# Performance work log

Measured on AMD Instinct MI355X. Metric: run time of the kernel, lower is better.

## Reference

```python
import jax, jax.numpy as jnp
import numpy as np
import math

B, N, K, C = 2, 8192, 16, 64
PE_DIM, HID = 32, 16
SIGMA, EPS = 1.0, 1e-06


def setup_inputs() -> dict:
    key = jax.random.key(0)
    ks = jax.random.split(key, 8)
    p = jax.random.normal(ks[0], (B, N, 3), jnp.float32)
    f = jax.random.normal(ks[1], (B, C, N), jnp.float32)
    pe = jax.random.normal(ks[2], (B, C, N, K), jnp.float32)
    knn_idx = jax.random.randint(ks[3], (B, N, K), 0, N, jnp.int32)
    # LocalAggregation convs1: 1x1 conv [C -> C] (+ReLU)
    W1 = jax.random.normal(ks[4], (C, C), jnp.float32) * (1.0 / math.sqrt(C))
    b1 = jnp.zeros((C,), jnp.float32)
    # GaussianKDEOffsetGenerator params: pe_mlp Linear(3->32), ffn Linear(32->16)->Linear(16->3)
    Wpe = jax.random.normal(ks[5], (PE_DIM, 3), jnp.float32) * (1.0 / math.sqrt(3))
    bpe = jnp.zeros((PE_DIM,), jnp.float32)
    Wh1 = jax.random.normal(ks[6], (HID, PE_DIM), jnp.float32) * (1.0 / math.sqrt(PE_DIM))
    bh1 = jnp.zeros((HID,), jnp.float32)
    Wh2 = jax.random.normal(ks[7], (3, HID), jnp.float32) * (1.0 / math.sqrt(HID))
    bh2 = jnp.zeros((3,), jnp.float32)
    return {"p": p, "f": f, "pe": pe, "W1": W1, "b1": b1, "Wpe": Wpe,
            "bpe": bpe, "Wh1": Wh1, "bh1": bh1, "Wh2": Wh2, "bh2": bh2,
            "knn_idx": knn_idx}


def reference(p, f, pe, W1, b1, Wpe, bpe, Wh1, bh1, Wh2, bh2, knn_idx):
    gather = jax.vmap(lambda a, i: a[i])  # per-batch neighbor gather
    # --- LocalAggregation: convs1 (1x1 conv + relu), group_by_idx, pe+fj, max-pool over K ---
    h = jax.nn.relu(jnp.einsum('oc,bcn->bon', W1, f) + b1[None, :, None])  # [B,C,N]
    ht = jnp.transpose(h, (0, 2, 1))                                       # [B,N,C]
    fj = gather(ht, knn_idx)                                               # [B,N,K,C]
    fout = jnp.max(pe + jnp.transpose(fj, (0, 3, 1, 2)), axis=-1)          # [B,C,N]
    # --- GaussianKDEOffsetGenerator on grouped neighbor coords [B*N, K, 3] ---
    coords = gather(p, knn_idx).reshape(B * N, K, 3)
    rel = coords[:, :, None, :] - coords[:, None, :, :]                    # [BN,K,K,3]
    pek = jax.nn.relu(jnp.einsum('nijc,dc->nijd', rel, Wpe) + bpe).mean(axis=2)  # [BN,K,PE]
    dist2 = jnp.sum(rel * rel, axis=-1)                                    # [BN,K,K]
    coef = 1.0 / math.sqrt(2.0 * math.pi * SIGMA ** 2 + EPS)
    kde = (coef * jnp.exp(-dist2 / (2.0 * SIGMA ** 2 + EPS))).sum(axis=2, keepdims=True)
    kde = kde / (jnp.max(kde, axis=1, keepdims=True) + EPS)                # [BN,K,1]
    fused = pek * kde
    delta = jax.nn.relu(fused @ Wh1.T + bh1) @ Wh2.T + bh2                 # [BN,K,3]
    return (fout, delta)
```

## Files before the change

### kernel.cpp

```cpp
#include <hip/hip_runtime.h>

#define B_ 2
#define N_ 8192
#define K_ 16
#define C_ 64
#define PE_ 32
#define HID_ 16

typedef float f4 __attribute__((ext_vector_type(4)));

__device__ __forceinline__ f4 splat4(float x) { f4 r = {x, x, x, x}; return r; }
__device__ __forceinline__ f4 relu4(f4 v) {
  f4 r;
  r[0] = fmaxf(v[0], 0.f); r[1] = fmaxf(v[1], 0.f);
  r[2] = fmaxf(v[2], 0.f); r[3] = fmaxf(v[3], 0.f);
  return r;
}
__device__ __forceinline__ float dot4(float4 w, f4 v) {
  return fmaf(w.x, v[0], fmaf(w.y, v[1], fmaf(w.z, v[2], w.w * v[3])));
}

struct PK4 { f4 k0, k1, k2, k3; };

__device__ __forceinline__ PK4 channel(const float4* __restrict__ sq,
                                       int d, const float* __restrict__ Wpe,
                                       const float* __restrict__ bpe) {
  const float wx = Wpe[d * 3 + 0], wy = Wpe[d * 3 + 1], wz = Wpe[d * 3 + 2];
  const float wb = bpe[d];
  const float4 A0 = sq[0], B0 = sq[1], C0 = sq[2];
  const float4 A1 = sq[3], B1 = sq[4], C1 = sq[5];
  const float4 A2 = sq[6], B2 = sq[7], C2 = sq[8];
  const float4 A3 = sq[9], B3 = sq[10], C3 = sq[11];
  const float p0  = fmaf(wx, A0.x, fmaf(wy, A0.y, wz * A0.z));
  const float p1  = fmaf(wx, A0.w, fmaf(wy, B0.x, wz * B0.y));
  const float p2  = fmaf(wx, B0.z, fmaf(wy, B0.w, wz * C0.x));
  const float p3  = fmaf(wx, C0.y, fmaf(wy, C0.z, wz * C0.w));
  const float p4  = fmaf(wx, A1.x, fmaf(wy, A1.y, wz * A1.z));
  const float p5  = fmaf(wx, A1.w, fmaf(wy, B1.x, wz * B1.y));
  const float p6  = fmaf(wx, B1.z, fmaf(wy, B1.w, wz * C1.x));
  const float p7  = fmaf(wx, C1.y, fmaf(wy, C1.z, wz * C1.w));
  const float p8  = fmaf(wx, A2.x, fmaf(wy, A2.y, wz * A2.z));
  const float p9  = fmaf(wx, A2.w, fmaf(wy, B2.x, wz * B2.y));
  const float p10 = fmaf(wx, B2.z, fmaf(wy, B2.w, wz * C2.x));
  const float p11 = fmaf(wx, C2.y, fmaf(wy, C2.z, wz * C2.w));
  const float p12 = fmaf(wx, A3.x, fmaf(wy, A3.y, wz * A3.z));
  const float p13 = fmaf(wx, A3.w, fmaf(wy, B3.x, wz * B3.y));
  const float p14 = fmaf(wx, B3.z, fmaf(wy, B3.w, wz * C3.x));
  const float p15 = fmaf(wx, C3.y, fmaf(wy, C3.z, wz * C3.w));
  const f4 a0 = {p0 + wb, p1 + wb, p2 + wb, p3 + wb};
  const f4 a1 = {p4 + wb, p5 + wb, p6 + wb, p7 + wb};
  const f4 a2 = {p8 + wb, p9 + wb, p10 + wb, p11 + wb};
  const f4 a3 = {p12 + wb, p13 + wb, p14 + wb, p15 + wb};
  f4 k0 = splat4(0.f), k1 = splat4(0.f), k2 = splat4(0.f), k3 = splat4(0.f);
#define KSTEP(PJ)                                  \
  {                                                \
    const f4 sp = splat4(PJ);                      \
    k0 += relu4(a0 - sp); k1 += relu4(a1 - sp);    \
    k2 += relu4(a2 - sp); k3 += relu4(a3 - sp);    \
  }
  KSTEP(p0) KSTEP(p1) KSTEP(p2) KSTEP(p3) KSTEP(p4) KSTEP(p5) KSTEP(p6)
  KSTEP(p7) KSTEP(p8) KSTEP(p9) KSTEP(p10) KSTEP(p11) KSTEP(p12) KSTEP(p13)
  KSTEP(p14) KSTEP(p15)
#undef KSTEP
  PK4 r; r.k0 = k0; r.k1 = k1; r.k2 = k2; r.k3 = k3;
  return r;
}

__global__ __launch_bounds__(256) void k1_conv(
    const float* __restrict__ f, const float* __restrict__ W1,
    const float* __restrict__ b1, float* __restrict__ ht) {
  const int t = threadIdx.x;
  const int lane = t & 63;
  const int w = t >> 6;
  const int g0 = blockIdx.x * 16 + w * 4;
  const int b = g0 >> 13;
  const int n = g0 & (N_ - 1);
  const f4* wp = reinterpret_cast<const f4*>(W1 + lane * C_);
  const f4 w0 = wp[0], w1 = wp[1], w2 = wp[2], w3 = wp[3];
  const f4 w4 = wp[4], w5 = wp[5], w6 = wp[6], w7 = wp[7];
  const f4 w8 = wp[8], w9 = wp[9], w10 = wp[10], w11 = wp[11];
  const f4 w12 = wp[12], w13 = wp[13], w14 = wp[14], w15 = wp[15];
  const float* fb = f + (size_t)b * C_ * N_ + n;
  f4 a = splat4(0.f);
#define CSTEP(Q, E)                                                        \
  {                                                                        \
    const f4 fv = *reinterpret_cast<const f4*>(fb + (size_t)(Q * 4 + E) * N_); \
    a += splat4(w##Q[E]) * fv;                                             \
  }
#define CQ(Q) CSTEP(Q, 0) CSTEP(Q, 1) CSTEP(Q, 2) CSTEP(Q, 3)
  CQ(0) CQ(1) CQ(2) CQ(3) CQ(4) CQ(5) CQ(6) CQ(7)
  CQ(8) CQ(9) CQ(10) CQ(11) CQ(12) CQ(13) CQ(14) CQ(15)
#undef CQ
#undef CSTEP
  const float bias = b1[lane];
  #pragma unroll
  for (int pt = 0; pt < 4; ++pt)
    ht[(size_t)(b * N_ + n + pt) * C_ + lane] = fmaxf(a[pt] + bias, 0.f);
}

#define SFJ_STRIDE 65
#define SOUT_OFF 16640
#define NP2 1024
__global__ __launch_bounds__(256) void k23_split(
    const float* __restrict__ p, const float* __restrict__ pe,
    const float* __restrict__ ht, const int* __restrict__ knn,
    const float* __restrict__ Wpe, const float* __restrict__ bpe,
    const float* __restrict__ Wh1, const float* __restrict__ bh1,
    const float* __restrict__ Wh2, const float* __restrict__ bh2,
    float* __restrict__ fout, float* __restrict__ delta) {
  __shared__ __align__(16) char smem[21760];
  const int t = threadIdx.x;

  if (blockIdx.x < NP2) {
    float* sfj = (float*)smem;
    float* sout = (float*)(smem + SOUT_OFF);
    const int base = blockIdx.x * 16;
    const int b = base >> 13;
    const int n0b = base & (N_ - 1);
    const int lane = t & 63;
    const int w = t >> 6;
    const int csub = lane >> 4, sl = lane & 15;
    const int j = sl & 3, nn = sl >> 2;
    #pragma unroll 1
    for (int si = 0; si < 4; ++si) {
      const int n0 = n0b + si * 4;
      #pragma unroll
      for (int n = 0; n < 4; ++n) {
        const int* kn = knn + (size_t)(b * N_ + n0 + n) * K_ + w * 4;
        #pragma unroll
        for (int kk = 0; kk < 4; ++kk) {
          const int id = kn[kk];
          const float hv = ht[(size_t)(b * N_ + id) * C_ + lane];
          sfj[lane * SFJ_STRIDE + (n * 4 + w) * 4 + kk] = hv;
        }
      }
      __syncthreads();
      #pragma unroll
      for (int it2 = 0; it2 < 4; ++it2) {
        const int c = it2 * 16 + w * 4 + csub;
        const f4 pv = __builtin_nontemporal_load(
            reinterpret_cast<const f4*>(pe + ((size_t)(b * C_ + c) * N_ + n0) * K_) + sl);
        const f4 fj = *reinterpret_cast<const f4*>(&sfj[c * SFJ_STRIDE + sl * 4]);
        float v = fmaxf(fmaxf(pv[0] + fj[0], pv[1] + fj[1]),
                        fmaxf(pv[2] + fj[2], pv[3] + fj[3]));
        v = fmaxf(v, __shfl_xor(v, 1));
        v = fmaxf(v, __shfl_xor(v, 2));
        if (j == 0) sout[c * 20 + si * 4 + nn] = v;
      }
      __syncthreads();
    }
    const int c = t >> 2, q = t & 3;
    const float4 r = *reinterpret_cast<const float4*>(&sout[c * 20 + q * 4]);
    *reinterpret_cast<float4*>(fout + (size_t)(b * C_ + c) * N_ + n0b + q * 4) = r;
    return;
  }

  {
    float* spk = (float*)smem;
    float* sc = (float*)(smem + 16384);
    const int base = (blockIdx.x - NP2) * 8;
    const int b = base >> 13;
    const int g = t >> 5;
    const int l = t & 31;

    if (l < 16) {
      const int gid = base + g;
      const int idx = knn[(size_t)gid * K_ + l];
      const float* pp = p + (size_t)(b * N_ + idx) * 3;
      sc[g * 48 + l * 3 + 0] = pp[0];
      sc[g * 48 + l * 3 + 1] = pp[1];
      sc[g * 48 + l * 3 + 2] = pp[2];
    }
    __syncthreads();

    {
      const int d = l;
      const float4* sq = reinterpret_cast<const float4*>(&sc[g * 48]);
      const PK4 ck = channel(sq, d, Wpe, bpe);
      const int qw = d >> 2, pos = d & 3;
      float* gbase = spk + g * 512;
#define PKW(II, KV) \
      gbase[(II) * 32 + (((qw ^ ((II) & 7)) << 2) | pos)] = ck.KV[(II) & 3];
      PKW(0, k0) PKW(1, k0) PKW(2, k0) PKW(3, k0)
      PKW(4, k1) PKW(5, k1) PKW(6, k1) PKW(7, k1)
      PKW(8, k2) PKW(9, k2) PKW(10, k2) PKW(11, k2)
      PKW(12, k3) PKW(13, k3) PKW(14, k3) PKW(15, k3)
#undef PKW
    }
    __syncthreads();

    {
      const int i = t & 15, half = (t >> 4) & 1;
      const int gid = base + g;
      const float ci0 = sc[g * 48 + i * 3 + 0];
      const float ci1 = sc[g * 48 + i * 3 + 1];
      const float ci2 = sc[g * 48 + i * 3 + 2];
      const float4* sq = reinterpret_cast<const float4*>(&sc[g * 48]);
      const float INV2S = 0.49999975f;
      const float COEF = 0.39894225f;
      float kacc = 0.f;
      #pragma unroll
      for (int jj = 0; jj < 2; ++jj) {
        const int j4 = half * 2 + jj;
        const float4 a = sq[j4 * 3 + 0], b4 = sq[j4 * 3 + 1], c4 = sq[j4 * 3 + 2];
        float dx, dy, dz;
        dx = ci0 - a.x;  dy = ci1 - a.y;  dz = ci2 - a.z;
        kacc += __expf(-(dx * dx + dy * dy + dz * dz) * INV2S);
        dx = ci0 - a.w;  dy = ci1 - b4.x; dz = ci2 - b4.y;
        kacc += __expf(-(dx * dx + dy * dy + dz * dz) * INV2S);
        dx = ci0 - b4.z; dy = ci1 - b4.w; dz = ci2 - c4.x;
        kacc += __expf(-(dx * dx + dy * dy + dz * dz) * INV2S);
        dx = ci0 - c4.y; dy = ci1 - c4.z; dz = ci2 - c4.w;
        kacc += __expf(-(dx * dx + dy * dy + dz * dz) * INV2S);
      }
      kacc += __shfl_xor(kacc, 16);
      const float kde = COEF * kacc;
      float m = kde;
      m = fmaxf(m, __shfl_xor(m, 1));
      m = fmaxf(m, __shfl_xor(m, 2));
      m = fmaxf(m, __shfl_xor(m, 4));
      m = fmaxf(m, __shfl_xor(m, 8));
      const float s = (kde / (m + 1e-6f)) * (1.f / 16.f);

      const float* rbase = spk + g * 512 + i * 32;
      const int ix = i & 7;
      const f4 v0 = *reinterpret_cast<const f4*>(&rbase[(0 ^ ix) << 2]);
      const f4 v1 = *reinterpret_cast<const f4*>(&rbase[(1 ^ ix) << 2]);
      const f4 v2 = *reinterpret_cast<const f4*>(&rbase[(2 ^ ix) << 2]);
      const f4 v3 = *reinterpret_cast<const f4*>(&rbase[(3 ^ ix) << 2]);
      const f4 v4 = *reinterpret_cast<const f4*>(&rbase[(4 ^ ix) << 2]);
      const f4 v5 = *reinterpret_cast<const f4*>(&rbase[(5 ^ ix) << 2]);
      const f4 v6 = *reinterpret_cast<const f4*>(&rbase[(6 ^ ix) << 2]);
      const f4 v7 = *reinterpret_cast<const f4*>(&rbase[(7 ^ ix) << 2]);

      float o0 = 0.f, o1 = 0.f, o2 = 0.f;
      #pragma unroll
      for (int hh = 0; hh < 8; ++hh) {
        const int h = half * 8 + hh;
        const float4* Wr = reinterpret_cast<const float4*>(Wh1 + h * PE_);
        const float u = dot4(Wr[0], v0) + dot4(Wr[1], v1) + dot4(Wr[2], v2) +
                        dot4(Wr[3], v3) + dot4(Wr[4], v4) + dot4(Wr[5], v5) +
                        dot4(Wr[6], v6) + dot4(Wr[7], v7);
        const float a = fmaxf(fmaf(s, u, bh1[h]), 0.f);
        o0 = fmaf(Wh2[0 * HID_ + h], a, o0);
        o1 = fmaf(Wh2[1 * HID_ + h], a, o1);
        o2 = fmaf(Wh2[2 * HID_ + h], a, o2);
      }
      o0 += __shfl_xor(o0, 16);
      o1 += __shfl_xor(o1, 16);
      o2 += __shfl_xor(o2, 16);
      if (half == 0) {
        float* dp = delta + ((size_t)gid * K_ + i) * 3;
        dp[0] = o0 + bh2[0];
        dp[1] = o1 + bh2[1];
        dp[2] = o2 + bh2[2];
      }
    }
  }
}

extern "C" void kernel_launch(void* const* d_in, const int* in_sizes, int n_in,
                              void* d_out, int out_size, void* d_ws, size_t ws_size,
                              hipStream_t stream) {
  const float* p   = (const float*)d_in[0];
  const float* f   = (const float*)d_in[1];
  const float* pe  = (const float*)d_in[2];
  const float* W1  = (const float*)d_in[3];
  const float* b1  = (const float*)d_in[4];
  const float* Wpe = (const float*)d_in[5];
  const float* bpe = (const float*)d_in[6];
  const float* Wh1 = (const float*)d_in[7];
  const float* bh1 = (const float*)d_in[8];
  const float* Wh2 = (const float*)d_in[9];
  const float* bh2 = (const float*)d_in[10];
  const int* knn   = (const int*)d_in[11];
  float* fout  = (float*)d_out;
  float* delta = (float*)d_out + (size_t)B_ * C_ * N_;
  float* ht = (float*)d_ws;

  k1_conv<<<(B_ * N_) / 16, 256, 0, stream>>>(f, W1, b1, ht);
  k23_split<<<NP2 + (B_ * N_) / 8, 256, 0, stream>>>(
      p, pe, ht, knn, Wpe, bpe, Wh1, bh1, Wh2, bh2, fout, delta);
}
```

Measured before the change: 65.99 us.

## Split KDE offset work across conv and gather kernels to balance launches

Restructures the two launches so the independent KDE/offset-MLP blocks are split between the first kernel (with the 1x1 conv) and the second kernel (with the neighbor gather and max-pool). The goal is to fill the conv kernel, which is lighter and bandwidth-bound, with compute work that does not depend on its output. That shortens the second kernel's tail. The first kernel now also allocates shared memory for the KDE blocks, and the fixed split ratio may not match the actual costs of each phase.

```diff
diff --git a/kernel.cpp b/kernel.cpp
--- a/kernel.cpp
+++ b/kernel.cpp
@@ -66,13 +66,12 @@
   return r;
 }
 
-__global__ __launch_bounds__(256) void k1_conv(
-    const float* __restrict__ f, const float* __restrict__ W1,
+__device__ __forceinline__ void k1_body(
+    int blk, int t, const float* __restrict__ f, const float* __restrict__ W1,
     const float* __restrict__ b1, float* __restrict__ ht) {
-  const int t = threadIdx.x;
   const int lane = t & 63;
   const int w = t >> 6;
-  const int g0 = blockIdx.x * 16 + w * 4;
+  const int g0 = blk * 16 + w * 4;
   const int b = g0 >> 13;
   const int n = g0 & (N_ - 1);
   const f4* wp = reinterpret_cast<const f4*>(W1 + lane * C_);
@@ -100,163 +99,193 @@
 
 #define SFJ_STRIDE 65
 #define SOUT_OFF 16640
-#define NP2 1024
-__global__ __launch_bounds__(256) void k23_split(
-    const float* __restrict__ p, const float* __restrict__ pe,
+__device__ __forceinline__ void p2_body(
+    char* smem, int blk, int t, const float* __restrict__ pe,
     const float* __restrict__ ht, const int* __restrict__ knn,
+    float* __restrict__ fout) {
+  float* sfj = (float*)smem;
+  float* sout = (float*)(smem + SOUT_OFF);
+  const int base = blk * 16;
+  const int b = base >> 13;
+  const int n0b = base & (N_ - 1);
+  const int lane = t & 63;
+  const int w = t >> 6;
+  const int csub = lane >> 4, sl = lane & 15;
+  const int j = sl & 3, nn = sl >> 2;
+  #pragma unroll 1
+  for (int si = 0; si < 4; ++si) {
+    const int n0 = n0b + si * 4;
+    #pragma unroll
+    for (int n = 0; n < 4; ++n) {
+      const int* kn = knn + (size_t)(b * N_ + n0 + n) * K_ + w * 4;
+      #pragma unroll
+      for (int kk = 0; kk < 4; ++kk) {
+        const int id = kn[kk];
+        const float hv = ht[(size_t)(b * N_ + id) * C_ + lane];
+        sfj[lane * SFJ_STRIDE + (n * 4 + w) * 4 + kk] = hv;
+      }
+    }
+    __syncthreads();
+    #pragma unroll
+    for (int it2 = 0; it2 < 4; ++it2) {
+      const int c = it2 * 16 + w * 4 + csub;
+      const f4 pv = __builtin_nontemporal_load(
+          reinterpret_cast<const f4*>(pe + ((size_t)(b * C_ + c) * N_ + n0) * K_) + sl);
+      const f4 fj = *reinterpret_cast<const f4*>(&sfj[c * SFJ_STRIDE + sl * 4]);
+      float v = fmaxf(fmaxf(pv[0] + fj[0], pv[1] + fj[1]),
+                      fmaxf(pv[2] + fj[2], pv[3] + fj[3]));
+      v = fmaxf(v, __shfl_xor(v, 1));
+      v = fmaxf(v, __shfl_xor(v, 2));
+      if (j == 0) sout[c * 20 + si * 4 + nn] = v;
+    }
+    __syncthreads();
+  }
+  const int c = t >> 2, q = t & 3;
+  const float4 r = *reinterpret_cast<const float4*>(&sout[c * 20 + q * 4]);
+  *reinterpret_cast<float4*>(fout + (size_t)(b * C_ + c) * N_ + n0b + q * 4) = r;
+}
+
+__device__ __forceinline__ void p3_body(
+    char* smem, int base, int t, const float* __restrict__ p,
+    const int* __restrict__ knn, const float* __restrict__ Wpe,
+    const float* __restrict__ bpe, const float* __restrict__ Wh1,
+    const float* __restrict__ bh1, const float* __restrict__ Wh2,
+    const float* __restrict__ bh2, float* __restrict__ delta) {
+  float* spk = (float*)smem;
+  float* sc = (float*)(smem + 16384);
+  const int b = base >> 13;
+  const int g = t >> 5;
+  const int l = t & 31;
+
+  if (l < 16) {
+    const int gid = base + g;
+    const int idx = knn[(size_t)gid * K_ + l];
+    const float* pp = p + (size_t)(b * N_ + idx) * 3;
+    sc[g * 48 + l * 3 + 0] = pp[0];
+    sc[g * 48 + l * 3 + 1] = pp[1];
+    sc[g * 48 + l * 3 + 2] = pp[2];
+  }
+  __syncthreads();
+
+  {
+    const int d = l;
+    const float4* sq = reinterpret_cast<const float4*>(&sc[g * 48]);
+    const PK4 ck = channel(sq, d, Wpe, bpe);
+    const int qw = d >> 2, pos = d & 3;
+    float* gbase = spk + g * 512;
+#define PKW(II, KV) \
+    gbase[(II) * 32 + (((qw ^ ((II) & 7)) << 2) | pos)] = ck.KV[(II) & 3];
+    PKW(0, k0) PKW(1, k0) PKW(2, k0) PKW(3, k0)
+    PKW(4, k1) PKW(5, k1) PKW(6, k1) PKW(7, k1)
+    PKW(8, k2) PKW(9, k2) PKW(10, k2) PKW(11, k2)
+    PKW(12, k3) PKW(13, k3) PKW(14, k3) PKW(15, k3)
+#undef PKW
+  }
+  __syncthreads();
+
+  {
+    const int i = t & 15, half = (t >> 4) & 1;
+    const int gid = base + g;
+    const float ci0 = sc[g * 48 + i * 3 + 0];
+    const float ci1 = sc[g * 48 + i * 3 + 1];
+    const float ci2 = sc[g * 48 + i * 3 + 2];
+    const float4* sq = reinterpret_cast<const float4*>(&sc[g * 48]);
+    const float INV2S = 0.49999975f;
+    const float COEF = 0.39894225f;
+    float kacc = 0.f;
+    #pragma unroll
+    for (int jj = 0; jj < 2; ++jj) {
+      const int j4 = half * 2 + jj;
+      const float4 a = sq[j4 * 3 + 0], b4 = sq[j4 * 3 + 1], c4 = sq[j4 * 3 + 2];
+      float dx, dy, dz;
+      dx = ci0 - a.x;  dy = ci1 - a.y;  dz = ci2 - a.z;
+      kacc += __expf(-(dx * dx + dy * dy + dz * dz) * INV2S);
+      dx = ci0 - a.w;  dy = ci1 - b4.x; dz = ci2 - b4.y;
+      kacc += __expf(-(dx * dx + dy * dy + dz * dz) * INV2S);
+      dx = ci0 - b4.z; dy = ci1 - b4.w; dz = ci2 - c4.x;
+      kacc += __expf(-(dx * dx + dy * dy + dz * dz) * INV2S);
+      dx = ci0 - c4.y; dy = ci1 - c4.z; dz = ci2 - c4.w;
+      kacc += __expf(-(dx * dx + dy * dy + dz * dz) * INV2S);
+    }
+    kacc += __shfl_xor(kacc, 16);
+    const float kde = COEF * kacc;
+    float m = kde;
+    m = fmaxf(m, __shfl_xor(m, 1));
+    m = fmaxf(m, __shfl_xor(m, 2));
+    m = fmaxf(m, __shfl_xor(m, 4));
+    m = fmaxf(m, __shfl_xor(m, 8));
+    const float s = (kde / (m + 1e-6f)) * (1.f / 16.f);
+
+    const float* rbase = spk + g * 512 + i * 32;
+    const int ix = i & 7;
+    const f4 v0 = *reinterpret_cast<const f4*>(&rbase[(0 ^ ix) << 2]);
+    const f4 v1 = *reinterpret_cast<const f4*>(&rbase[(1 ^ ix) << 2]);
+    const f4 v2 = *reinterpret_cast<const f4*>(&rbase[(2 ^ ix) << 2]);
+    const f4 v3 = *reinterpret_cast<const f4*>(&rbase[(3 ^ ix) << 2]);
+    const f4 v4 = *reinterpret_cast<const f4*>(&rbase[(4 ^ ix) << 2]);
+    const f4 v5 = *reinterpret_cast<const f4*>(&rbase[(5 ^ ix) << 2]);
+    const f4 v6 = *reinterpret_cast<const f4*>(&rbase[(6 ^ ix) << 2]);
+    const f4 v7 = *reinterpret_cast<const f4*>(&rbase[(7 ^ ix) << 2]);
+
+    float o0 = 0.f, o1 = 0.f, o2 = 0.f;
+    #pragma unroll
+    for (int hh = 0; hh < 8; ++hh) {
+      const int h = half * 8 + hh;
+      const float4* Wr = reinterpret_cast<const float4*>(Wh1 + h * PE_);
+      const float u = dot4(Wr[0], v0) + dot4(Wr[1], v1) + dot4(Wr[2], v2) +
+                      dot4(Wr[3], v3) + dot4(Wr[4], v4) + dot4(Wr[5], v5) +
+                      dot4(Wr[6], v6) + dot4(Wr[7], v7);
+      const float a = fmaxf(fmaf(s, u, bh1[h]), 0.f);
+      o0 = fmaf(Wh2[0 * HID_ + h], a, o0);
+      o1 = fmaf(Wh2[1 * HID_ + h], a, o1);
+      o2 = fmaf(Wh2[2 * HID_ + h], a, o2);
+    }
+    o0 += __shfl_xor(o0, 16);
+    o1 += __shfl_xor(o1, 16);
+    o2 += __shfl_xor(o2, 16);
+    if (half == 0) {
+      float* dp = delta + ((size_t)gid * K_ + i) * 3;
+      dp[0] = o0 + bh2[0];
+      dp[1] = o1 + bh2[1];
+      dp[2] = o2 + bh2[2];
+    }
+  }
+}
+
+#define NP3A 1280
+__global__ __launch_bounds__(256) void kA(
+    const float* __restrict__ f, const float* __restrict__ W1,
+    const float* __restrict__ b1, float* __restrict__ ht,
+    const float* __restrict__ p, const int* __restrict__ knn,
     const float* __restrict__ Wpe, const float* __restrict__ bpe,
     const float* __restrict__ Wh1, const float* __restrict__ bh1,
     const float* __restrict__ Wh2, const float* __restrict__ bh2,
-    float* __restrict__ fout, float* __restrict__ delta) {
+    float* __restrict__ delta) {
+  __shared__ __align__(16) char smem[17920];
+  const int t = threadIdx.x;
+  if (blockIdx.x < 1024) {
+    k1_body(blockIdx.x, t, f, W1, b1, ht);
+    return;
+  }
+  p3_body(smem, (blockIdx.x - 1024) * 8, t, p, knn, Wpe, bpe, Wh1, bh1,
+          Wh2, bh2, delta);
+}
+
+__global__ __launch_bounds__(256) void kB(
+    const float* __restrict__ pe, const float* __restrict__ ht,
+    const int* __restrict__ knn, float* __restrict__ fout,
+    const float* __restrict__ p, const float* __restrict__ Wpe,
+    const float* __restrict__ bpe, const float* __restrict__ Wh1,
+    const float* __restrict__ bh1, const float* __restrict__ Wh2,
+    const float* __restrict__ bh2, float* __restrict__ delta) {
   __shared__ __align__(16) char smem[21760];
   const int t = threadIdx.x;
-
-  if (blockIdx.x < NP2) {
-    float* sfj = (float*)smem;
-    float* sout = (float*)(smem + SOUT_OFF);
-    const int base = blockIdx.x * 16;
-    const int b = base >> 13;
-    const int n0b = base & (N_ - 1);
-    const int lane = t & 63;
-    const int w = t >> 6;
-    const int csub = lane >> 4, sl = lane & 15;
-    const int j = sl & 3, nn = sl >> 2;
-    #pragma unroll 1
-    for (int si = 0; si < 4; ++si) {
-      const int n0 = n0b + si * 4;
-      #pragma unroll
-      for (int n = 0; n < 4; ++n) {
-        const int* kn = knn + (size_t)(b * N_ + n0 + n) * K_ + w * 4;
-        #pragma unroll
-        for (int kk = 0; kk < 4; ++kk) {
-          const int id = kn[kk];
-          const float hv = ht[(size_t)(b * N_ + id) * C_ + lane];
-          sfj[lane * SFJ_STRIDE + (n * 4 + w) * 4 + kk] = hv;
-        }
-      }
-      __syncthreads();
-      #pragma unroll
-      for (int it2 = 0; it2 < 4; ++it2) {
-        const int c = it2 * 16 + w * 4 + csub;
-        const f4 pv = __builtin_nontemporal_load(
-            reinterpret_cast<const f4*>(pe + ((size_t)(b * C_ + c) * N_ + n0) * K_) + sl);
-        const f4 fj = *reinterpret_cast<const f4*>(&sfj[c * SFJ_STRIDE + sl * 4]);
-        float v = fmaxf(fmaxf(pv[0] + fj[0], pv[1] + fj[1]),
-                        fmaxf(pv[2] + fj[2], pv[3] + fj[3]));
-        v = fmaxf(v, __shfl_xor(v, 1));
-        v = fmaxf(v, __shfl_xor(v, 2));
-        if (j == 0) sout[c * 20 + si * 4 + nn] = v;
-      }
-      __syncthreads();
-    }
-    const int c = t >> 2, q = t & 3;
-    const float4 r = *reinterpret_cast<const float4*>(&sout[c * 20 + q * 4]);
-    *reinterpret_cast<float4*>(fout + (size_t)(b * C_ + c) * N_ + n0b + q * 4) = r;
+  if (blockIdx.x < 1024) {
+    p2_body(smem, blockIdx.x, t, pe, ht, knn, fout);
     return;
   }
-
-  {
-    float* spk = (float*)smem;
-    float* sc = (float*)(smem + 16384);
-    const int base = (blockIdx.x - NP2) * 8;
-    const int b = base >> 13;
-    const int g = t >> 5;
-    const int l = t & 31;
-
-    if (l < 16) {
-      const int gid = base + g;
-      const int idx = knn[(size_t)gid * K_ + l];
-      const float* pp = p + (size_t)(b * N_ + idx) * 3;
-      sc[g * 48 + l * 3 + 0] = pp[0];
-      sc[g * 48 + l * 3 + 1] = pp[1];
-      sc[g * 48 + l * 3 + 2] = pp[2];
-    }
-    __syncthreads();
-
-    {
-      const int d = l;
-      const float4* sq = reinterpret_cast<const float4*>(&sc[g * 48]);
-      const PK4 ck = channel(sq, d, Wpe, bpe);
-      const int qw = d >> 2, pos = d & 3;
-      float* gbase = spk + g * 512;
-#define PKW(II, KV) \
-      gbase[(II) * 32 + (((qw ^ ((II) & 7)) << 2) | pos)] = ck.KV[(II) & 3];
-      PKW(0, k0) PKW(1, k0) PKW(2, k0) PKW(3, k0)
-      PKW(4, k1) PKW(5, k1) PKW(6, k1) PKW(7, k1)
-      PKW(8, k2) PKW(9, k2) PKW(10, k2) PKW(11, k2)
-      PKW(12, k3) PKW(13, k3) PKW(14, k3) PKW(15, k3)
-#undef PKW
-    }
-    __syncthreads();
-
-    {
-      const int i = t & 15, half = (t >> 4) & 1;
-      const int gid = base + g;
-      const float ci0 = sc[g * 48 + i * 3 + 0];
-      const float ci1 = sc[g * 48 + i * 3 + 1];
-      const float ci2 = sc[g * 48 + i * 3 + 2];
-      const float4* sq = reinterpret_cast<const float4*>(&sc[g * 48]);
-      const float INV2S = 0.49999975f;
-      const float COEF = 0.39894225f;
-      float kacc = 0.f;
-      #pragma unroll
-      for (int jj = 0; jj < 2; ++jj) {
-        const int j4 = half * 2 + jj;
-        const float4 a = sq[j4 * 3 + 0], b4 = sq[j4 * 3 + 1], c4 = sq[j4 * 3 + 2];
-        float dx, dy, dz;
-        dx = ci0 - a.x;  dy = ci1 - a.y;  dz = ci2 - a.z;
-        kacc += __expf(-(dx * dx + dy * dy + dz * dz) * INV2S);
-        dx = ci0 - a.w;  dy = ci1 - b4.x; dz = ci2 - b4.y;
-        kacc += __expf(-(dx * dx + dy * dy + dz * dz) * INV2S);
-        dx = ci0 - b4.z; dy = ci1 - b4.w; dz = ci2 - c4.x;
-        kacc += __expf(-(dx * dx + dy * dy + dz * dz) * INV2S);
-        dx = ci0 - c4.y; dy = ci1 - c4.z; dz = ci2 - c4.w;
-        kacc += __expf(-(dx * dx + dy * dy + dz * dz) * INV2S);
-      }
-      kacc += __shfl_xor(kacc, 16);
-      const float kde = COEF * kacc;
-      float m = kde;
-      m = fmaxf(m, __shfl_xor(m, 1));
-      m = fmaxf(m, __shfl_xor(m, 2));
-      m = fmaxf(m, __shfl_xor(m, 4));
-      m = fmaxf(m, __shfl_xor(m, 8));
-      const float s = (kde / (m + 1e-6f)) * (1.f / 16.f);
-
-      const float* rbase = spk + g * 512 + i * 32;
-      const int ix = i & 7;
-      const f4 v0 = *reinterpret_cast<const f4*>(&rbase[(0 ^ ix) << 2]);
-      const f4 v1 = *reinterpret_cast<const f4*>(&rbase[(1 ^ ix) << 2]);
-      const f4 v2 = *reinterpret_cast<const f4*>(&rbase[(2 ^ ix) << 2]);
-      const f4 v3 = *reinterpret_cast<const f4*>(&rbase[(3 ^ ix) << 2]);
-      const f4 v4 = *reinterpret_cast<const f4*>(&rbase[(4 ^ ix) << 2]);
-      const f4 v5 = *reinterpret_cast<const f4*>(&rbase[(5 ^ ix) << 2]);
-      const f4 v6 = *reinterpret_cast<const f4*>(&rbase[(6 ^ ix) << 2]);
-      const f4 v7 = *reinterpret_cast<const f4*>(&rbase[(7 ^ ix) << 2]);
-
-      float o0 = 0.f, o1 = 0.f, o2 = 0.f;
-      #pragma unroll
-      for (int hh = 0; hh < 8; ++hh) {
-        const int h = half * 8 + hh;
-        const float4* Wr = reinterpret_cast<const float4*>(Wh1 + h * PE_);
-        const float u = dot4(Wr[0], v0) + dot4(Wr[1], v1) + dot4(Wr[2], v2) +
-                        dot4(Wr[3], v3) + dot4(Wr[4], v4) + dot4(Wr[5], v5) +
-                        dot4(Wr[6], v6) + dot4(Wr[7], v7);
-        const float a = fmaxf(fmaf(s, u, bh1[h]), 0.f);
-        o0 = fmaf(Wh2[0 * HID_ + h], a, o0);
-        o1 = fmaf(Wh2[1 * HID_ + h], a, o1);
-        o2 = fmaf(Wh2[2 * HID_ + h], a, o2);
-      }
-      o0 += __shfl_xor(o0, 16);
-      o1 += __shfl_xor(o1, 16);
-      o2 += __shfl_xor(o2, 16);
-      if (half == 0) {
-        float* dp = delta + ((size_t)gid * K_ + i) * 3;
-        dp[0] = o0 + bh2[0];
-        dp[1] = o1 + bh2[1];
-        dp[2] = o2 + bh2[2];
-      }
-    }
-  }
+  p3_body(smem, NP3A * 8 + (blockIdx.x - 1024) * 8, t, p, knn, Wpe, bpe,
+          Wh1, bh1, Wh2, bh2, delta);
 }
 
 extern "C" void kernel_launch(void* const* d_in, const int* in_sizes, int n_in,
@@ -278,7 +307,8 @@
   float* delta = (float*)d_out + (size_t)B_ * C_ * N_;
   float* ht = (float*)d_ws;
 
-  k1_conv<<<(B_ * N_) / 16, 256, 0, stream>>>(f, W1, b1, ht);
-  k23_split<<<NP2 + (B_ * N_) / 8, 256, 0, stream>>>(
-      p, pe, ht, knn, Wpe, bpe, Wh1, bh1, Wh2, bh2, fout, delta);
-}
+  kA<<<1024 + NP3A, 256, 0, stream>>>(f, W1, b1, ht, p, knn, Wpe, bpe,
+                                      Wh1, bh1, Wh2, bh2, delta);
+  kB<<<1024 + ((B_ * N_ / 8) - NP3A), 256, 0, stream>>>(
+      pe, ht, knn, fout, p, Wpe, bpe, Wh1, bh1, Wh2, bh2, delta);
+}
```

Measured after the change: 67.61 us. +2.5%, slower.
